# Kernel optimization log

Hardware: AMD Instinct MI355X
Metric: run time of the kernel (lower is better)

Reference implementation:

```python
import jax, jax.numpy as jnp
import numpy as np

SIZE = (160, 192, 160)  # D, H, W


def _warp(x, flow):
    """Faithful port of SpatialTransformer.forward (3D, trilinear, align_corners=True,
    zeros padding). Normalization to [-1,1] followed by grid_sample's denormalization
    cancels exactly, so sample positions are grid + flow in voxel coordinates."""
    B, C, D, H, W = x.shape
    f32 = x.dtype
    gz, gy, gx = jnp.meshgrid(
        jnp.arange(D, dtype=f32), jnp.arange(H, dtype=f32), jnp.arange(W, dtype=f32),
        indexing='ij')
    # sample positions per voxel, [B, D, H, W]
    pz = gz[None] + flow[:, 0]
    py = gy[None] + flow[:, 1]
    px = gx[None] + flow[:, 2]

    z0 = jnp.floor(pz); y0 = jnp.floor(py); x0 = jnp.floor(px)
    fz = pz - z0; fy = py - y0; fx = px - x0
    z0i = z0.astype(jnp.int32); y0i = y0.astype(jnp.int32); x0i = x0.astype(jnp.int32)

    x_flat = x.reshape(B, C, D * H * W)
    out = jnp.zeros_like(x)
    for dz in (0, 1):
        zi = z0i + dz
        wz = fz if dz else (1.0 - fz)
        mz = (zi >= 0) & (zi < D)
        zc = jnp.clip(zi, 0, D - 1)
        for dy in (0, 1):
            yi = y0i + dy
            wy = fy if dy else (1.0 - fy)
            my = (yi >= 0) & (yi < H)
            yc = jnp.clip(yi, 0, H - 1)
            for dx in (0, 1):
                xi = x0i + dx
                wx = fx if dx else (1.0 - fx)
                mx = (xi >= 0) & (xi < W)
                xc = jnp.clip(xi, 0, W - 1)
                # zeros padding: clip index for gather, zero the weight if OOB
                w = (wz * wy * wx) * (mz & my & mx).astype(f32)  # [B,D,H,W]
                flat = ((zc * H + yc) * W + xc).reshape(B, 1, D * H * W)
                g = jnp.take_along_axis(x_flat, flat, axis=2).reshape(B, C, D, H, W)
                out = out + g * w[:, None]
    return out


def setup_inputs() -> dict:
    key = jax.random.key(0)
    k1, k2 = jax.random.split(key)
    x = jax.random.normal(k1, (2, 2) + SIZE, dtype=jnp.float32)
    flow = jax.random.normal(k2, (2, 3) + SIZE, dtype=jnp.float32)
    return {"x": x, "flow": flow}


def reference(x, flow):
    return _warp(x, flow)
```

## Files before the change

kernel.cpp:

```cpp
#include <hip/hip_runtime.h>
#include <hip/hip_fp16.h>

#define DD 160
#define HH 192
#define WW 160
#define VOL (DD * HH * WW)
#define NB 2
#define NC 2

#define TZ 8
#define TY 8
#define TX 16
#define NTZ (DD / TZ)
#define NTY (HH / TY)
#define NTX (WW / TX)
#define TPB (NTZ * NTY * NTX)
#define NBLK (NB * TPB)
#define NXCD 8

#define HLO 3
#define HHI 4
#define RZM (TZ + HLO + HHI)
#define RYM (TY + HLO + HHI)
#define RXP 28
#define ZSTR (RYM * RXP)
#define CSTR (RZM * ZSTR)

typedef float    v4f  __attribute__((ext_vector_type(4)));
typedef unsigned v4u  __attribute__((ext_vector_type(4)));
typedef float    v2fu __attribute__((ext_vector_type(2), aligned(4)));

__global__ __launch_bounds__(256, 6) void warp_kernel(
    const float* __restrict__ x,
    const float* __restrict__ flow,
    float* __restrict__ out)
{
    __shared__ unsigned lds[CSTR];

    int bid = blockIdx.x;
    int vid = (bid & (NXCD - 1)) * (NBLK / NXCD) + (bid >> 3);

    int b  = vid / TPB;
    int r  = vid - b * TPB;
    int tz = r / (NTY * NTX);
    int r2 = r - tz * (NTY * NTX);
    int ty = r2 / NTX;
    int tx = r2 - ty * NTX;

    int oz = tz * TZ, oy = ty * TY, ox = tx * TX;

    int bz0 = max(oz - HLO, 0), bz1 = min(oz + TZ + HHI, DD);
    int by0 = max(oy - HLO, 0), by1 = min(oy + TY + HHI, HH);
    int bx0 = max(ox - HLO, 0) & ~3;
    int bx1 = min(ox + TX + HHI, WW);
    int RZ = bz1 - bz0, RY = by1 - by0;

    int tid = threadIdx.x;

    {
        int lane8 = tid & 7, rowid = tid >> 3;
        int nrows = RZ * RYM;
        const size_t LIM = (size_t)NB * NC * VOL - 4;
        if (lane8 < 7) {
            for (int rr = rowid; rr < nrows; rr += 32) {
                int z = rr / RYM;
                int y = rr - z * RYM;
                if (y < RY) {
                    size_t g0 = (size_t)b * NC * VOL
                              + (size_t)((bz0 + z) * HH + (by0 + y)) * WW
                              + (size_t)(bx0 + lane8 * 4);
                    size_t g1 = g0 + VOL;
                    if (g0 > LIM) g0 = LIM;
                    if (g1 > LIM) g1 = LIM;
                    v4f a0 = *(const v4f*)(x + g0);
                    v4f a1 = *(const v4f*)(x + g1);
                    v4u pk;
#pragma unroll
                    for (int q = 0; q < 4; ++q) {
                        __half2 h = __halves2half2(__float2half(a0[q]),
                                                   __float2half(a1[q]));
                        pk[q] = __builtin_bit_cast(unsigned, h);
                    }
                    *(v4u*)(lds + z * ZSTR + y * RXP + lane8 * 4) = pk;
                }
            }
        }
    }
    __syncthreads();

    const float* fb  = flow + (size_t)b * 3 * VOL;
    const float* xb0 = x + (size_t)b * NC * VOL;
    const float* xb1 = xb0 + VOL;
    float* ob        = out + (size_t)b * NC * VOL;

#pragma unroll
    for (int i = 0; i < 4; ++i) {
        int V  = tid + 256 * i;
        int xl = V & 15, yl = (V >> 4) & 7, zl = V >> 7;
        int gz = oz + zl, gy = oy + yl, gx = ox + xl;
        int gi = (gz * HH + gy) * WW + gx;

        float dzf = __builtin_nontemporal_load(fb + gi);
        float dyf = __builtin_nontemporal_load(fb + gi + VOL);
        float dxf = __builtin_nontemporal_load(fb + gi + 2 * VOL);

        float pz = gz + dzf, py = gy + dyf, px = gx + dxf;

        float z0f = floorf(pz), y0f = floorf(py), x0f = floorf(px);
        float fz = pz - z0f, fy = py - y0f, fx = px - x0f;
        int z0 = (int)z0f, y0 = (int)y0f, x0 = (int)x0f;
        int z1 = z0 + 1,  y1 = y0 + 1,  x1 = x0 + 1;

        float wz0 = (z0 >= 0 && z0 < DD) ? (1.0f - fz) : 0.0f;
        float wz1 = (z1 >= 0 && z1 < DD) ? fz : 0.0f;
        float wy0 = (y0 >= 0 && y0 < HH) ? (1.0f - fy) : 0.0f;
        float wy1 = (y1 >= 0 && y1 < HH) ? fy : 0.0f;
        float wx0 = (x0 >= 0 && x0 < WW) ? (1.0f - fx) : 0.0f;
        float wx1 = (x1 >= 0 && x1 < WW) ? fx : 0.0f;

        int z0c = min(max(z0, 0), DD - 1);
        int z1c = min(max(z1, 0), DD - 1);
        int y0c = min(max(y0, 0), HH - 1);
        int y1c = min(max(y1, 0), HH - 1);
        int x0c = min(max(x0, 0), WW - 1);
        int x1c = min(max(x1, 0), WW - 1);

        int base = min(x0c, WW - 2);

        float a  = ((x0c == base) ? wx0 : 0.0f) + ((x1c == base) ? wx1 : 0.0f);
        float bb = (wx0 + wx1) - a;

        float w0 = wz0 * wy0, w1 = wz0 * wy1, w2 = wz1 * wy0, w3 = wz1 * wy1;
        float wA0 = w0 * a,  wB0 = w0 * bb;
        float wA1 = w1 * a,  wB1 = w1 * bb;
        float wA2 = w2 * a,  wB2 = w2 * bb;
        float wA3 = w3 * a,  wB3 = w3 * bb;

        bool inbox = (z0c >= bz0) && (z1c < bz1) &&
                     (y0c >= by0) && (y1c < by1) &&
                     (base >= bx0) && (base + 1 < bx1);

        float s0, s1;
        if (inbox) {
            int lx  = base - bx0;
            int A00 = (z0c - bz0) * ZSTR + (y0c - by0) * RXP + lx;
            int A01 = (z0c - bz0) * ZSTR + (y1c - by0) * RXP + lx;
            int A10 = (z1c - bz0) * ZSTR + (y0c - by0) * RXP + lx;
            int A11 = (z1c - bz0) * ZSTR + (y1c - by0) * RXP + lx;
            s0 = 0.0f; s1 = 0.0f;
#pragma unroll
            for (int k = 0; k < 4; ++k) {
                int   A  = (k == 0) ? A00 : (k == 1) ? A01 : (k == 2) ? A10 : A11;
                float wa = (k == 0) ? wA0 : (k == 1) ? wA1 : (k == 2) ? wA2 : wA3;
                float wb = (k == 0) ? wB0 : (k == 1) ? wB1 : (k == 2) ? wB2 : wB3;
                unsigned m0 = lds[A];
                unsigned m1 = lds[A + 1];
                float2 f0 = __half22float2(__builtin_bit_cast(__half2, m0));
                float2 f1 = __half22float2(__builtin_bit_cast(__half2, m1));
                s0 += wa * f0.x + wb * f1.x;
                s1 += wa * f0.y + wb * f1.y;
            }
        } else {
            int p00 = (z0c * HH + y0c) * WW + base;
            int p01 = (z0c * HH + y1c) * WW + base;
            int p10 = (z1c * HH + y0c) * WW + base;
            int p11 = (z1c * HH + y1c) * WW + base;
            v2fu c;
            s0 = 0.0f; s1 = 0.0f;
            c = *(const v2fu*)(xb0 + p00); s0 += wA0 * c.x + wB0 * c.y;
            c = *(const v2fu*)(xb0 + p01); s0 += wA1 * c.x + wB1 * c.y;
            c = *(const v2fu*)(xb0 + p10); s0 += wA2 * c.x + wB2 * c.y;
            c = *(const v2fu*)(xb0 + p11); s0 += wA3 * c.x + wB3 * c.y;
            c = *(const v2fu*)(xb1 + p00); s1 += wA0 * c.x + wB0 * c.y;
            c = *(const v2fu*)(xb1 + p01); s1 += wA1 * c.x + wB1 * c.y;
            c = *(const v2fu*)(xb1 + p10); s1 += wA2 * c.x + wB2 * c.y;
            c = *(const v2fu*)(xb1 + p11); s1 += wA3 * c.x + wB3 * c.y;
        }

        __builtin_nontemporal_store(s0, ob + gi);
        __builtin_nontemporal_store(s1, ob + gi + VOL);
    }
}

extern "C" void kernel_launch(void* const* d_in, const int* in_sizes, int n_in,
                              void* d_out, int out_size, void* d_ws, size_t ws_size,
                              hipStream_t stream) {
    const float* x    = (const float*)d_in[0];
    const float* flow = (const float*)d_in[1];
    float* out        = (float*)d_out;

    warp_kernel<<<NBLK, 256, 0, stream>>>(x, flow, out);
}
```

Before: 294.6 us.

## Prefetch flow before LDS staging, shrink halo tile, raise occupancy bound

Flow loads for all four voxels per thread are issued before the shared-memory halo fill, so their latency overlaps with the x staging loads and the barrier. The LDS row pitch drops from 28 to 24 words, which still covers the 4-aligned x halo, and the staging loop is unrolled with a fixed row count and no per-row bounds check. Launch bounds go from 6 to 8 blocks per CU so more blocks fit. In exchange the kernel holds 12 extra live registers across the barrier, and boundary tiles now read unused rows beyond the volume edge.

```diff
diff --git a/kernel.cpp b/kernel.cpp
--- a/kernel.cpp
+++ b/kernel.cpp
@@ -18,19 +18,19 @@
 #define NBLK (NB * TPB)
 #define NXCD 8
 
-#define HLO 3
-#define HHI 4
-#define RZM (TZ + HLO + HHI)
-#define RYM (TY + HLO + HHI)
-#define RXP 28
+#define RZM 15
+#define RYM 15
+#define RXP 24
 #define ZSTR (RYM * RXP)
 #define CSTR (RZM * ZSTR)
+
+#define NROWS (RZM * RYM)
 
 typedef float    v4f  __attribute__((ext_vector_type(4)));
 typedef unsigned v4u  __attribute__((ext_vector_type(4)));
 typedef float    v2fu __attribute__((ext_vector_type(2), aligned(4)));
 
-__global__ __launch_bounds__(256, 6) void warp_kernel(
+__global__ __launch_bounds__(256, 8) void warp_kernel(
     const float* __restrict__ x,
     const float* __restrict__ flow,
     float* __restrict__ out)
@@ -49,23 +49,41 @@
 
     int oz = tz * TZ, oy = ty * TY, ox = tx * TX;
 
-    int bz0 = max(oz - HLO, 0), bz1 = min(oz + TZ + HHI, DD);
-    int by0 = max(oy - HLO, 0), by1 = min(oy + TY + HHI, HH);
-    int bx0 = max(ox - HLO, 0) & ~3;
-    int bx1 = min(ox + TX + HHI, WW);
-    int RZ = bz1 - bz0, RY = by1 - by0;
+    int bz0 = max(oz - 3, 0), bz1 = min(oz + TZ + 4, DD);
+    int by0 = max(oy - 3, 0), by1 = min(oy + TY + 4, HH);
+    int bx0 = max(ox - 3, 0) & ~3;
+    int bx1 = min(ox + TX + 4, WW);
 
     int tid = threadIdx.x;
+
+    const float* fb  = flow + (size_t)b * 3 * VOL;
+    const float* xb0 = x + (size_t)b * NC * VOL;
+    const float* xb1 = xb0 + VOL;
+    float* ob        = out + (size_t)b * NC * VOL;
+
+    float pfz[4], pfy[4], pfx[4];
+    int   gidx[4];
+#pragma unroll
+    for (int i = 0; i < 4; ++i) {
+        int V  = tid + 256 * i;
+        int xl = V & 15, yl = (V >> 4) & 7, zl = V >> 7;
+        int gi = ((oz + zl) * HH + (oy + yl)) * WW + (ox + xl);
+        gidx[i] = gi;
+        pfz[i] = __builtin_nontemporal_load(fb + gi);
+        pfy[i] = __builtin_nontemporal_load(fb + gi + VOL);
+        pfx[i] = __builtin_nontemporal_load(fb + gi + 2 * VOL);
+    }
 
     {
         int lane8 = tid & 7, rowid = tid >> 3;
-        int nrows = RZ * RYM;
         const size_t LIM = (size_t)NB * NC * VOL - 4;
-        if (lane8 < 7) {
-            for (int rr = rowid; rr < nrows; rr += 32) {
-                int z = rr / RYM;
-                int y = rr - z * RYM;
-                if (y < RY) {
+        if (lane8 < 6) {
+#pragma unroll
+            for (int k = 0; k < 8; ++k) {
+                int rr = rowid + 32 * k;
+                if (rr < NROWS) {
+                    int z = rr / RYM;
+                    int y = rr - z * RYM;
                     size_t g0 = (size_t)b * NC * VOL
                               + (size_t)((bz0 + z) * HH + (by0 + y)) * WW
                               + (size_t)(bx0 + lane8 * 4);
@@ -88,23 +106,14 @@
     }
     __syncthreads();
 
-    const float* fb  = flow + (size_t)b * 3 * VOL;
-    const float* xb0 = x + (size_t)b * NC * VOL;
-    const float* xb1 = xb0 + VOL;
-    float* ob        = out + (size_t)b * NC * VOL;
-
 #pragma unroll
     for (int i = 0; i < 4; ++i) {
         int V  = tid + 256 * i;
         int xl = V & 15, yl = (V >> 4) & 7, zl = V >> 7;
         int gz = oz + zl, gy = oy + yl, gx = ox + xl;
-        int gi = (gz * HH + gy) * WW + gx;
-
-        float dzf = __builtin_nontemporal_load(fb + gi);
-        float dyf = __builtin_nontemporal_load(fb + gi + VOL);
-        float dxf = __builtin_nontemporal_load(fb + gi + 2 * VOL);
-
-        float pz = gz + dzf, py = gy + dyf, px = gx + dxf;
+        int gi = gidx[i];
+
+        float pz = gz + pfz[i], py = gy + pfy[i], px = gx + pfx[i];
 
         float z0f = floorf(pz), y0f = floorf(py), x0f = floorf(px);
         float fz = pz - z0f, fy = py - y0f, fx = px - x0f;
```

Result: no change. 289.2 us (-1.9%).
